# Kernel tuning notes

Hardware: AMD Instinct MI355X
Metric: run time of the kernel (lower is better)

## Reference

```python
import jax, jax.numpy as jnp
import numpy as np

NUM_TOKENS = 8192
TOKEN_DIM = 256
COMMITMENT_COST = 0.25
BATCH, SEQ = 32, 1024


def setup_inputs() -> dict:
    key = jax.random.key(0)
    k_z, k_cb = jax.random.split(key)
    z = jax.random.normal(k_z, (BATCH, SEQ, TOKEN_DIM), dtype=jnp.float32)
    # nn.Parameter(torch.randn(num_tokens, token_dim) * 0.02)
    codebook = jax.random.normal(k_cb, (NUM_TOKENS, TOKEN_DIM), dtype=jnp.float32) * 0.02
    return {"z": z, "codebook": codebook}


def reference(z, codebook):
    """VQ forward (eval mode): cdist^2 + argmin + gather + straight-through + commitment loss.

    z:        (B, S, D) continuous features
    codebook: (K, D) codebook vectors
    Returns (z_q, token_ids, loss) matching AudioCodebook.forward.
    """
    B, S, D = z.shape
    z_flat = z.reshape(-1, D)  # (N, D)
    # squared euclidean distances: ||z||^2 - 2 z.c^T + ||c||^2  -> (N, K)
    distances = (
        jnp.sum(z_flat * z_flat, axis=1, keepdims=True)
        - 2.0 * jnp.matmul(z_flat, codebook.T)
        + jnp.sum(codebook * codebook, axis=1)[None, :]
    )
    token_ids = jnp.argmin(distances, axis=-1)  # (N,)
    z_q = codebook[token_ids]  # (N, D) gather
    # straight-through estimator
    z_q_flat = z_flat + jax.lax.stop_gradient(z_q - z_flat)
    # commitment loss: mse(z_q_flat, stop_grad(z_flat))
    diff = z_q_flat - jax.lax.stop_gradient(z_flat)
    loss = COMMITMENT_COST * jnp.mean(diff * diff)
    return z_q_flat.reshape(B, S, D), token_ids.reshape(B, S), loss
```

## Files before the change

kernel.cpp:

```cpp
#include <hip/hip_runtime.h>
#include <math.h>

#define NTOK 32768
#define DIM 256
#define KCB 8192
#define RESCUE_TAU 4e-3f
#define RPASS 8

typedef _Float16 half8 __attribute__((ext_vector_type(8)));
typedef float f32x4 __attribute__((ext_vector_type(4)));
typedef unsigned long long u64;
typedef unsigned int u32;

#define OFF_AN    0ull
#define OFF_CN    131072ull
#define OFF_IDS   163840ull
#define OFF_RCNT  294912ull
#define OFF_RLIST 295040ull
#define OFF_PART  426112ull
#define OFF_PK1   442496ull
#define OFF_PV2   2539648ull
#define OFF_Z16   3588224ull
#define OFF_CB16  37142656ull
#define WS_NEED   45531264ull

#define GLOAD_LDS16(gp, lp) __builtin_amdgcn_global_load_lds( \
    (const __attribute__((address_space(1))) void*)(gp), \
    (__attribute__((address_space(3))) void*)(lp), 16, 0, 0)

static __device__ __forceinline__ u64 umin64(u64 a, u64 b) { return a < b ? a : b; }
static __device__ __forceinline__ u64 umax64(u64 a, u64 b) { return a < b ? b : a; }

__global__ __launch_bounds__(256)
void rownorm256_np(const float* __restrict__ M, float* __restrict__ out, int rows) {
  int r = blockIdx.x * 256 + threadIdx.x;
  if (r >= rows) return;
  const float* p = M + (size_t)r * DIM;
  float blk[2];
#pragma unroll
  for (int b = 0; b < 2; ++b) {
    const float* a = p + b * 128;
    float rr[8];
#pragma unroll
    for (int j = 0; j < 8; ++j) rr[j] = __fmul_rn(a[j], a[j]);
    for (int i = 8; i < 128; i += 8) {
#pragma unroll
      for (int j = 0; j < 8; ++j)
        rr[j] = __fadd_rn(rr[j], __fmul_rn(a[i + j], a[i + j]));
    }
    float s01 = __fadd_rn(rr[0], rr[1]);
    float s23 = __fadd_rn(rr[2], rr[3]);
    float s45 = __fadd_rn(rr[4], rr[5]);
    float s67 = __fadd_rn(rr[6], rr[7]);
    blk[b] = __fadd_rn(__fadd_rn(s01, s23), __fadd_rn(s45, s67));
  }
  out[r] = __fadd_rn(blk[0], blk[1]);
}

__global__ __launch_bounds__(128)
void conv_z16(const float* __restrict__ z, _Float16* __restrict__ dst) {
  const int tile = blockIdx.x >> 3, ks = blockIdx.x & 7, row = threadIdx.x;
  const float* src = z + ((size_t)(tile * 128 + row)) * DIM + ks * 32;
  _Float16* d = dst + (u64)tile * 65536 + (u64)ks * 8192 + row * 64;
  const int rs = row & 7;
#pragma unroll
  for (int q = 0; q < 4; ++q) {
    half8 hv, lv;
#pragma unroll
    for (int j = 0; j < 8; ++j) {
      float f = src[q * 8 + j] * 64.0f;
      _Float16 h = (_Float16)f;
      float lf = f - (float)h;
      hv[j] = h; lv[j] = (_Float16)lf;
    }
    *reinterpret_cast<half8*>(d + ((q ^ rs) * 8)) = hv;
    *reinterpret_cast<half8*>(d + (((q + 4) ^ rs) * 8)) = lv;
  }
}

__global__ __launch_bounds__(256)
void conv_cb16(const float* __restrict__ cb, _Float16* __restrict__ dst) {
  const int tile = blockIdx.x >> 3, ks = blockIdx.x & 7, row = threadIdx.x;
  const float* src = cb + ((size_t)(tile * 256 + row)) * DIM + ks * 32;
  _Float16* d = dst + (u64)tile * 131072 + (u64)ks * 16384 + row * 64;
  const int rs = row & 7;
#pragma unroll
  for (int q = 0; q < 4; ++q) {
    half8 hv, lv;
#pragma unroll
    for (int j = 0; j < 8; ++j) {
      float f = src[q * 8 + j] * 1024.0f;
      _Float16 h = (_Float16)f;
      float lf = f - (float)h;
      hv[j] = h; lv[j] = (_Float16)lf;
    }
    *reinterpret_cast<half8*>(d + ((q ^ rs) * 8)) = hv;
    *reinterpret_cast<half8*>(d + (((q + 4) ^ rs) * 8)) = lv;
  }
}

__global__ __launch_bounds__(256, 3)
void vq_mfma_top2(const _Float16* __restrict__ z16, const _Float16* __restrict__ cb16,
                  const float* __restrict__ An, const float* __restrict__ Cn,
                  u64* __restrict__ pk1, float* __restrict__ pv2) {
  __shared__ _Float16 Bs0[128 * 64];
  __shared__ _Float16 Bs1[128 * 64];
  __shared__ float    Cs[1024];
  __shared__ u64      t2k[64][2];
  __shared__ u32      t2v[64][2];

  const int tid = threadIdx.x;
  const int lane = tid & 63, w = tid >> 6;
  const int wm = w >> 1, wn = w & 1;
  const int swz = (blockIdx.x & 7) * 512 + (blockIdx.x >> 3);
  const int cg = swz >> 9, rem = swz & 511;
  const int ttile = rem >> 1, thalf = rem & 1;
  const int laneM = lane & 15, laneK = lane >> 4;
  const _Float16* zt = z16 + (u64)ttile * 65536;

  int offA[2];
#pragma unroll
  for (int f = 0; f < 2; ++f) {
    int row = thalf * 64 + wm * 32 + f * 16 + laneM;
    offA[f] = row * 64 + ((laneK ^ (row & 7)) * 8);
  }
  int offBh[4], offBl[4];
#pragma unroll
  for (int g = 0; g < 4; ++g) {
    int row = wn * 64 + g * 16 + laneM;
    offBh[g] = row * 64 + ((laneK ^ (row & 7)) * 8);
    offBl[g] = row * 64 + (((laneK + 4) ^ (row & 7)) * 8);
  }

  half8 Ah[8][2];
#pragma unroll
  for (int ks = 0; ks < 8; ++ks)
#pragma unroll
    for (int f = 0; f < 2; ++f)
      Ah[ks][f] = *reinterpret_cast<const half8*>(zt + ks * 8192 + offA[f]);

  float Areg[2][4];
#pragma unroll
  for (int f = 0; f < 2; ++f) {
    float4 a4 = *reinterpret_cast<const float4*>(
        &An[ttile * 128 + thalf * 64 + wm * 32 + f * 16 + laneK * 4]);
    Areg[f][0] = a4.x; Areg[f][1] = a4.y; Areg[f][2] = a4.z; Areg[f][3] = a4.w;
  }
  {
    float4 c4 = *reinterpret_cast<const float4*>(&Cn[cg * 1024 + tid * 4]);
    *reinterpret_cast<float4*>(&Cs[tid * 4]) = c4;
  }

  u32 v1b[8], v2b[8], c1v[8];
#pragma unroll
  for (int s = 0; s < 8; ++s) { v1b[s] = 0x7F800000u; v2b[s] = 0x7F800000u; c1v[s] = 0; }
  u32 codeSub = (u32)(cg * 1024 + wn * 64 + laneM);

#define STAGE_B(s, Bd) do {                                                  \
    const int ns_ = (s) >> 3, nk_ = (s) & 7;                                 \
    const _Float16* sb_ = cb16 + (u64)(cg * 4 + (ns_ >> 1)) * 131072 +       \
                          (u64)nk_ * 16384 + (u64)(ns_ & 1) * 8192 + tid * 8;\
    GLOAD_LDS16(sb_,        &Bd[tid * 8]);                                   \
    GLOAD_LDS16(sb_ + 2048, &Bd[tid * 8 + 2048]);                            \
    GLOAD_LDS16(sb_ + 4096, &Bd[tid * 8 + 4096]);                            \
    GLOAD_LDS16(sb_ + 6144, &Bd[tid * 8 + 6144]);                            \
  } while (0)

#define COMPUTE_KS(kc, Bsrc) do {                                            \
    _Pragma("unroll")                                                        \
    for (int g_ = 0; g_ < 4; ++g_) {                                         \
      half8 bh = *reinterpret_cast<const half8*>(&Bsrc[offBh[g_]]);          \
      half8 bl = *reinterpret_cast<const half8*>(&Bsrc[offBl[g_]]);          \
      _Pragma("unroll")                                                      \
      for (int f_ = 0; f_ < 2; ++f_)                                         \
        acc[f_][g_] = __builtin_amdgcn_mfma_f32_16x16x32_f16(Ah[kc][f_], bh, acc[f_][g_], 0, 0, 0); \
      _Pragma("unroll")                                                      \
      for (int f_ = 0; f_ < 2; ++f_)                                         \
        acc[f_][g_] = __builtin_amdgcn_mfma_f32_16x16x32_f16(Ah[kc][f_], bl, acc[f_][g_], 0, 0, 0); \
    }                                                                        \
  } while (0)

  STAGE_B(0, Bs0);
  __syncthreads();

  f32x4 acc[2][4];
#pragma unroll
  for (int f = 0; f < 2; ++f)
#pragma unroll
    for (int g = 0; g < 4; ++g) acc[f][g] = (f32x4){0.f, 0.f, 0.f, 0.f};

  for (int sub = 0; sub < 8; ++sub) {
#pragma unroll
    for (int ks = 0; ks < 8; ++ks) {
      const int step = sub * 8 + ks;
      if (step < 63) {
        if (ks & 1) STAGE_B(step + 1, Bs0);
        else        STAGE_B(step + 1, Bs1);
      }
      if (ks & 1) COMPUTE_KS(ks, Bs1);
      else        COMPUTE_KS(ks, Bs0);

      if (ks == 7) {
        const int cbase = sub * 128 + wn * 64 + laneM;
        float Cg[4];
#pragma unroll
        for (int g = 0; g < 4; ++g) Cg[g] = Cs[cbase + g * 16];
#pragma unroll
        for (int f = 0; f < 2; ++f) {
#pragma unroll
          for (int r = 0; r < 4; ++r) {
            const int sl = f * 4 + r;
            const float Ar = Areg[f][r];
#pragma unroll
            for (int g = 0; g < 4; ++g) {
              float p2 = __fmul_rn(acc[f][g][r], 0x1p-15f);
              float t1 = __fsub_rn(Ar, p2);
              float t  = __fadd_rn(t1, Cg[g]);
              u32 tb = __float_as_uint(t);
              u32 code = codeSub + (u32)(g * 16);
              bool lt1 = tb < v1b[sl];
              bool lt2 = tb < v2b[sl];
              v2b[sl] = lt1 ? v1b[sl] : (lt2 ? tb : v2b[sl]);
              c1v[sl] = lt1 ? code : c1v[sl];
              v1b[sl] = lt1 ? tb : v1b[sl];
            }
          }
        }
        codeSub += 128;
#pragma unroll
        for (int f = 0; f < 2; ++f)
#pragma unroll
          for (int g = 0; g < 4; ++g) acc[f][g] = (f32x4){0.f, 0.f, 0.f, 0.f};
      }
      __syncthreads();
    }
  }

#undef STAGE_B
#undef COMPUTE_KS

#pragma unroll
  for (int sl = 0; sl < 8; ++sl) {
#pragma unroll
    for (int d = 1; d < 16; d <<= 1) {
      u32 o1 = (u32)__shfl_xor((int)v1b[sl], d);
      u32 oc = (u32)__shfl_xor((int)c1v[sl], d);
      u32 o2 = (u32)__shfl_xor((int)v2b[sl], d);
      u64 k  = ((u64)v1b[sl] << 32) | c1v[sl];
      u64 ko = ((u64)o1 << 32) | oc;
      u32 loser = v1b[sl] < o1 ? o1 : v1b[sl];
      u32 nv2 = min(loser, min(v2b[sl], o2));
      u64 nk = umin64(k, ko);
      v1b[sl] = (u32)(nk >> 32); c1v[sl] = (u32)nk; v2b[sl] = nv2;
    }
  }
  if (laneM == 0) {
#pragma unroll
    for (int f = 0; f < 2; ++f)
#pragma unroll
      for (int r = 0; r < 4; ++r) {
        const int tloc = wm * 32 + f * 16 + laneK * 4 + r;
        const int sl = f * 4 + r;
        t2k[tloc][wn] = ((u64)v1b[sl] << 32) | c1v[sl];
        t2v[tloc][wn] = v2b[sl];
      }
  }
  __syncthreads();
  if (tid < 64) {
    u64 k0 = t2k[tid][0], k1 = t2k[tid][1];
    u32 va = t2v[tid][0], vb = t2v[tid][1];
    u64 K1 = umin64(k0, k1);
    u32 loser = (u32)(umax64(k0, k1) >> 32);
    u32 V2 = min(min(va, vb), loser);
    const int token = ttile * 128 + thalf * 64 + tid;
    pk1[(size_t)token * 8 + cg] = K1;
    pv2[(size_t)token * 8 + cg] = __uint_as_float(V2);
  }
}

__global__ __launch_bounds__(256)
void vq_detect(const u64* __restrict__ pk1, const float* __restrict__ pv2,
               int* __restrict__ ids, int* __restrict__ rcnt, int* __restrict__ rlist) {
  const int token = blockIdx.x * 256 + threadIdx.x;
  u64 K1 = pk1[(size_t)token * 8];
  float V2 = pv2[(size_t)token * 8];
#pragma unroll
  for (int c = 1; c < 8; ++c) {
    u64 k1 = pk1[(size_t)token * 8 + c];
    float v2 = pv2[(size_t)token * 8 + c];
    u64 n1 = (k1 < K1) ? k1 : K1;
    u64 hi = (k1 < K1) ? K1 : k1;
    float loser = __uint_as_float((unsigned)(hi >> 32));
    V2 = fminf(fminf(V2, v2), loser);
    K1 = n1;
  }
  ids[token] = (int)(K1 & 0xffffffffull);
  float d1 = __uint_as_float((unsigned)(K1 >> 32));
  if (V2 - d1 < RESCUE_TAU) {
    int p = atomicAdd(rcnt, 1);
    rlist[p] = token;
  }
}

__global__ __launch_bounds__(256)
void vq_rescue(const float* __restrict__ z, const float* __restrict__ cb,
               const float* __restrict__ An, const float* __restrict__ Cn,
               const int* __restrict__ rcnt, const int* __restrict__ rlist,
               int* __restrict__ ids) {
  __shared__ float zrow[RPASS][256];
  __shared__ u64 red[256];
  const int tid = threadIdx.x;
  const int total = *rcnt;
  for (int base = blockIdx.x * RPASS; base < total; base += gridDim.x * RPASS) {
    const int np = min(RPASS, total - base);
    __syncthreads();
    for (int li = tid; li < np * 256; li += 256)
      zrow[li >> 8][li & 255] = z[(size_t)rlist[base + (li >> 8)] * DIM + (li & 255)];
    __syncthreads();
    float Atok[RPASS];
#pragma unroll
    for (int s = 0; s < RPASS; ++s) Atok[s] = (s < np) ? An[rlist[base + s]] : 0.f;
    u64 bkey[RPASS];
#pragma unroll
    for (int s = 0; s < RPASS; ++s) bkey[s] = ~0ull;
    for (int jj = 0; jj < KCB / 256; ++jj) {
      const int j = jj * 256 + tid;
      const float4* crow = reinterpret_cast<const float4*>(cb + (size_t)j * DIM);
      float dots[RPASS];
#pragma unroll
      for (int s = 0; s < RPASS; ++s) dots[s] = 0.f;
      for (int k4 = 0; k4 < 64; ++k4) {
        const float4 c4 = crow[k4];
#pragma unroll
        for (int s = 0; s < RPASS; ++s) {
          const float4 z4 = *reinterpret_cast<const float4*>(&zrow[s][k4 * 4]);
          dots[s] = fmaf(z4.x, c4.x, dots[s]);
          dots[s] = fmaf(z4.y, c4.y, dots[s]);
          dots[s] = fmaf(z4.z, c4.z, dots[s]);
          dots[s] = fmaf(z4.w, c4.w, dots[s]);
        }
      }
      const float Cj = Cn[j];
#pragma unroll
      for (int s = 0; s < RPASS; ++s) {
        float p2 = __fmul_rn(2.0f, dots[s]);
        float t1 = __fsub_rn(Atok[s], p2);
        float t  = __fadd_rn(t1, Cj);
        u64 key = ((u64)__float_as_uint(t) << 32) | (u64)j;
        if (key < bkey[s]) bkey[s] = key;
      }
    }
    for (int s = 0; s < np; ++s) {
      __syncthreads();
      red[tid] = bkey[s];
      __syncthreads();
      for (int off = 128; off > 0; off >>= 1) {
        if (tid < off) { u64 o = red[tid + off]; if (o < red[tid]) red[tid] = o; }
        __syncthreads();
      }
      if (tid == 0) ids[rlist[base + s]] = (int)(red[0] & 0xffffffffull);
    }
  }
}

__global__ __launch_bounds__(256)
void vq_finalize_ids(const float* __restrict__ z, const float* __restrict__ cb,
                     const int* __restrict__ ids, float* __restrict__ out,
                     double* __restrict__ part) {
  __shared__ double sred[4];
  const int g64 = threadIdx.x >> 6, lane = threadIdx.x & 63;
  double s = 0.0;
#pragma unroll
  for (int i = 0; i < 4; ++i) {
    const int n = blockIdx.x * 16 + i * 4 + g64;
    const int bk = ids[n];
    const float4 c4 = *reinterpret_cast<const float4*>(&cb[(size_t)bk * DIM + lane * 4]);
    const float4 z4 = *reinterpret_cast<const float4*>(&z[(size_t)n * DIM + lane * 4]);
    *reinterpret_cast<float4*>(&out[(size_t)n * DIM + lane * 4]) = c4;
    float dx = __fsub_rn(c4.x, z4.x), dy = __fsub_rn(c4.y, z4.y);
    float dz = __fsub_rn(c4.z, z4.z), dw = __fsub_rn(c4.w, z4.w);
    s += (double)dx * dx + (double)dy * dy + (double)dz * dz + (double)dw * dw;
    if (lane == 0) out[(size_t)NTOK * DIM + n] = (float)bk;
  }
#pragma unroll
  for (int off = 32; off > 0; off >>= 1) s += __shfl_down(s, off);
  if (lane == 0) sred[g64] = s;
  __syncthreads();
  if (threadIdx.x == 0)
    part[blockIdx.x] = (sred[0] + sred[1]) + (sred[2] + sred[3]);
}

__global__ __launch_bounds__(256)
void vq_loss_write(const double* __restrict__ part, float* __restrict__ out) {
  __shared__ double red[256];
  double s = 0.0;
  for (int i = threadIdx.x; i < 2048; i += 256) s += part[i];
  red[threadIdx.x] = s;
  __syncthreads();
  for (int off = 128; off > 0; off >>= 1) {
    if (threadIdx.x < off) red[threadIdx.x] += red[threadIdx.x + off];
    __syncthreads();
  }
  if (threadIdx.x == 0)
    out[(size_t)NTOK * DIM + NTOK] =
        (float)(0.25 * red[0] / (double)((size_t)NTOK * DIM));
}

#define NCHUNK 8
#define CHUNK 1024
#define TT 128
#define CT 128
#define DC 32

__global__ __launch_bounds__(256)
void vq_argmin_kernel(const float* __restrict__ z, const float* __restrict__ cb,
                      const float* __restrict__ An, const float* __restrict__ Cn,
                      float* __restrict__ pv, int* __restrict__ pk) {
  __shared__ float zs[DC * TT];
  __shared__ float cs[DC * CT];
  const int tid = threadIdx.x;
  const int tx = tid & 15, ty = tid >> 4;
  const int chunk = blockIdx.x & 7;
  const int tile = blockIdx.x >> 3;
  const int base_t = tile * TT;
  const int base_k = chunk * CHUNK;
  float Areg[8];
#pragma unroll
  for (int i = 0; i < 8; ++i) Areg[i] = An[base_t + ty * 8 + i];
  float bestv[8]; int bestk[8];
#pragma unroll
  for (int i = 0; i < 8; ++i) { bestv[i] = INFINITY; bestk[i] = 0; }
  for (int st = 0; st < CHUNK / CT; ++st) {
    const int kb0 = base_k + st * CT;
    float acc[8][8];
#pragma unroll
    for (int i = 0; i < 8; ++i)
#pragma unroll
      for (int j = 0; j < 8; ++j) acc[i][j] = 0.f;
    for (int dc = 0; dc < DIM / DC; ++dc) {
      __syncthreads();
#pragma unroll
      for (int li = tid; li < DC * TT / 4; li += 256) {
        const int row = li >> 3;
        const int dv = li & 7;
        const int ibase = dv * 4 * 128 + (row ^ (dv << 2) ^ ((row & 32) >> 3));
        float4 v = *reinterpret_cast<const float4*>(
            &z[(size_t)(base_t + row) * DIM + dc * DC + dv * 4]);
        zs[ibase] = v.x; zs[ibase + 128] = v.y;
        zs[ibase + 256] = v.z; zs[ibase + 384] = v.w;
        float4 c = *reinterpret_cast<const float4*>(
            &cb[(size_t)(kb0 + row) * DIM + dc * DC + dv * 4]);
        cs[ibase] = c.x; cs[ibase + 128] = c.y;
        cs[ibase + 256] = c.z; cs[ibase + 384] = c.w;
      }
      __syncthreads();
#pragma unroll
      for (int dd = 0; dd < DC / 4; ++dd) {
        const int s1 = dd << 2;
        const float* zp0 = &zs[dd * 4 * 128 + ((ty * 8) ^ s1 ^ (ty & 4))];
        const float* zp1 = &zs[dd * 4 * 128 + ((ty * 8 + 4) ^ s1 ^ (ty & 4))];
        const float* cp0 = &cs[dd * 4 * 128 + ((tx * 8) ^ s1 ^ (tx & 4))];
        const float* cp1 = &cs[dd * 4 * 128 + ((tx * 8 + 4) ^ s1 ^ (tx & 4))];
#pragma unroll
        for (int q = 0; q < 4; ++q) {
          const float4 za  = *reinterpret_cast<const float4*>(zp0 + q * 128);
          const float4 zb  = *reinterpret_cast<const float4*>(zp1 + q * 128);
          const float4 ca  = *reinterpret_cast<const float4*>(cp0 + q * 128);
          const float4 cbv = *reinterpret_cast<const float4*>(cp1 + q * 128);
          const float zv[8] = {za.x, za.y, za.z, za.w, zb.x, zb.y, zb.z, zb.w};
          const float cv[8] = {ca.x, ca.y, ca.z, ca.w, cbv.x, cbv.y, cbv.z, cbv.w};
#pragma unroll
          for (int i = 0; i < 8; ++i)
#pragma unroll
            for (int j = 0; j < 8; ++j)
              acc[i][j] = fmaf(zv[i], cv[j], acc[i][j]);
        }
      }
    }
#pragma unroll
    for (int j = 0; j < 8; ++j) {
      const int klocal = st * CT + tx * 8 + j;
      const float Ck = Cn[base_k + klocal];
#pragma unroll
      for (int i = 0; i < 8; ++i) {
        float p2 = __fmul_rn(2.0f, acc[i][j]);
        float t1 = __fsub_rn(Areg[i], p2);
        float t  = __fadd_rn(t1, Ck);
        if (t < bestv[i]) { bestv[i] = t; bestk[i] = klocal; }
      }
    }
  }
  __syncthreads();
  float (*mv)[16] = reinterpret_cast<float(*)[16]>(zs);
  int   (*mk)[16] = reinterpret_cast<int(*)[16]>(zs + TT * 16);
#pragma unroll
  for (int i = 0; i < 8; ++i) { mv[ty * 8 + i][tx] = bestv[i]; mk[ty * 8 + i][tx] = bestk[i]; }
  __syncthreads();
  if (tid < TT) {
    float bv = mv[tid][0]; int bk = mk[tid][0];
#pragma unroll
    for (int x = 1; x < 16; ++x) {
      float v = mv[tid][x]; int k = mk[tid][x];
      if (v < bv || (v == bv && k < bk)) { bv = v; bk = k; }
    }
    size_t idx = (size_t)(base_t + tid) * NCHUNK + chunk;
    pv[idx] = bv;
    pk[idx] = base_k + bk;
  }
}

__global__ __launch_bounds__(256)
void vq_finalize(const float* __restrict__ z, const float* __restrict__ cb,
                 const float* __restrict__ pv, const int* __restrict__ pk,
                 float* __restrict__ out, double* __restrict__ loss_acc) {
  const int n = blockIdx.x * 4 + (threadIdx.x >> 6);
  const int lane = threadIdx.x & 63;
  float bv = INFINITY; int bk = 0;
#pragma unroll
  for (int c = 0; c < NCHUNK; ++c) {
    float v = pv[(size_t)n * NCHUNK + c];
    int k = pk[(size_t)n * NCHUNK + c];
    if (v < bv || (v == bv && k < bk)) { bv = v; bk = k; }
  }
  const float4 c4 = *reinterpret_cast<const float4*>(&cb[(size_t)bk * DIM + lane * 4]);
  const float4 z4 = *reinterpret_cast<const float4*>(&z[(size_t)n * DIM + lane * 4]);
  *reinterpret_cast<float4*>(&out[(size_t)n * DIM + lane * 4]) = c4;
  float dx = __fsub_rn(c4.x, z4.x), dy = __fsub_rn(c4.y, z4.y);
  float dz = __fsub_rn(c4.z, z4.z), dw = __fsub_rn(c4.w, z4.w);
  double s = (double)dx * dx + (double)dy * dy + (double)dz * dz + (double)dw * dw;
#pragma unroll
  for (int off = 32; off > 0; off >>= 1) s += __shfl_down(s, off);
  if (lane == 0) {
    out[(size_t)NTOK * DIM + n] = (float)bk;
    atomicAdd(loss_acc, s);
  }
}

__global__ void vq_loss_write_fb(const double* __restrict__ loss_acc, float* __restrict__ out) {
  out[(size_t)NTOK * DIM + NTOK] = (float)(0.25 * (*loss_acc) / (double)((size_t)NTOK * DIM));
}

extern "C" void kernel_launch(void* const* d_in, const int* in_sizes, int n_in,
                              void* d_out, int out_size, void* d_ws, size_t ws_size,
                              hipStream_t stream) {
  const float* z  = (const float*)d_in[0];
  const float* cb = (const float*)d_in[1];
  float* out = (float*)d_out;
  char* ws = (char*)d_ws;

  if (ws_size >= WS_NEED) {
    float*     An   = (float*)(ws + OFF_AN);
    float*     Cn   = (float*)(ws + OFF_CN);
    int*       ids  = (int*)(ws + OFF_IDS);
    int*       rcnt = (int*)(ws + OFF_RCNT);
    int*       rlist= (int*)(ws + OFF_RLIST);
    double*    part = (double*)(ws + OFF_PART);
    u64*       pk1  = (u64*)(ws + OFF_PK1);
    float*     pv2  = (float*)(ws + OFF_PV2);
    _Float16*  z16  = (_Float16*)(ws + OFF_Z16);
    _Float16*  c16  = (_Float16*)(ws + OFF_CB16);

    hipMemsetAsync(rcnt, 0, 128, stream);
    rownorm256_np<<<NTOK / 256, 256, 0, stream>>>(z, An, NTOK);
    rownorm256_np<<<KCB / 256, 256, 0, stream>>>(cb, Cn, KCB);
    conv_z16<<<256 * 8, 128, 0, stream>>>(z, z16);
    conv_cb16<<<32 * 8, 256, 0, stream>>>(cb, c16);
    vq_mfma_top2<<<4096, 256, 0, stream>>>(z16, c16, An, Cn, pk1, pv2);
    vq_detect<<<NTOK / 256, 256, 0, stream>>>(pk1, pv2, ids, rcnt, rlist);
    vq_rescue<<<1024, 256, 0, stream>>>(z, cb, An, Cn, rcnt, rlist, ids);
    vq_finalize_ids<<<NTOK / 16, 256, 0, stream>>>(z, cb, ids, out, part);
    vq_loss_write<<<1, 256, 0, stream>>>(part, out);
  } else {
    float*  An = (float*)(ws);
    float*  Cn = (float*)(ws + 131072);
    float*  pv = (float*)(ws + 163840);
    int*    pk = (int*)(ws + 1212416);
    double* loss = (double*)(ws + 2260992);
    hipMemsetAsync(loss, 0, sizeof(double), stream);
    rownorm256_np<<<NTOK / 256, 256, 0, stream>>>(z, An, NTOK);
    rownorm256_np<<<KCB / 256, 256, 0, stream>>>(cb, Cn, KCB);
    vq_argmin_kernel<<<(NTOK / TT) * NCHUNK, 256, 0, stream>>>(z, cb, An, Cn, pv, pk);
    vq_finalize<<<NTOK / 4, 256, 0, stream>>>(z, cb, pv, pk, out, loss);
    vq_loss_write_fb<<<1, 1, 0, stream>>>(loss, out);
  }
}
```

Measured before the change: 689.4 us.

## Split rescue pass across codebook chunks with wave-shuffle reduction and atomicMin

```diff
diff --git a/kernel.cpp b/kernel.cpp
--- a/kernel.cpp
+++ b/kernel.cpp
@@ -5,7 +5,6 @@
 #define DIM 256
 #define KCB 8192
 #define RESCUE_TAU 4e-3f
-#define RPASS 8
 
 typedef _Float16 half8 __attribute__((ext_vector_type(8)));
 typedef float f32x4 __attribute__((ext_vector_type(4)));
@@ -303,63 +302,65 @@
 }
 
 __global__ __launch_bounds__(256)
-void vq_rescue(const float* __restrict__ z, const float* __restrict__ cb,
-               const float* __restrict__ An, const float* __restrict__ Cn,
-               const int* __restrict__ rcnt, const int* __restrict__ rlist,
-               int* __restrict__ ids) {
-  __shared__ float zrow[RPASS][256];
-  __shared__ u64 red[256];
+void vq_rescue2(const float* __restrict__ z, const float* __restrict__ cb,
+                const float* __restrict__ An, const float* __restrict__ Cn,
+                const int* __restrict__ rcnt, const int* __restrict__ rlist,
+                u64* __restrict__ rmin) {
   const int tid = threadIdx.x;
   const int total = *rcnt;
-  for (int base = blockIdx.x * RPASS; base < total; base += gridDim.x * RPASS) {
-    const int np = min(RPASS, total - base);
-    __syncthreads();
-    for (int li = tid; li < np * 256; li += 256)
-      zrow[li >> 8][li & 255] = z[(size_t)rlist[base + (li >> 8)] * DIM + (li & 255)];
-    __syncthreads();
-    float Atok[RPASS];
-#pragma unroll
-    for (int s = 0; s < RPASS; ++s) Atok[s] = (s < np) ? An[rlist[base + s]] : 0.f;
-    u64 bkey[RPASS];
-#pragma unroll
-    for (int s = 0; s < RPASS; ++s) bkey[s] = ~0ull;
-    for (int jj = 0; jj < KCB / 256; ++jj) {
-      const int j = jj * 256 + tid;
-      const float4* crow = reinterpret_cast<const float4*>(cb + (size_t)j * DIM);
-      float dots[RPASS];
-#pragma unroll
-      for (int s = 0; s < RPASS; ++s) dots[s] = 0.f;
-      for (int k4 = 0; k4 < 64; ++k4) {
-        const float4 c4 = crow[k4];
-#pragma unroll
-        for (int s = 0; s < RPASS; ++s) {
-          const float4 z4 = *reinterpret_cast<const float4*>(&zrow[s][k4 * 4]);
-          dots[s] = fmaf(z4.x, c4.x, dots[s]);
-          dots[s] = fmaf(z4.y, c4.y, dots[s]);
-          dots[s] = fmaf(z4.z, c4.z, dots[s]);
-          dots[s] = fmaf(z4.w, c4.w, dots[s]);
-        }
-      }
-      const float Cj = Cn[j];
-#pragma unroll
-      for (int s = 0; s < RPASS; ++s) {
+  if (total == 0) return;
+  const int nb = (total + 31) >> 5;
+  for (int wi = blockIdx.x; wi < nb * 32; wi += gridDim.x) {
+    const int batch = wi >> 5, chunk = wi & 31;
+    const int base = batch * 32;
+    const int np = min(32, total - base);
+    int toks[32];
+#pragma unroll
+    for (int s = 0; s < 32; ++s)
+      toks[s] = rlist[base + (s < np ? s : 0)];
+    const int j = chunk * 256 + tid;
+    const float4* crow = reinterpret_cast<const float4*>(cb + (size_t)j * DIM);
+    float dots[32];
+#pragma unroll
+    for (int s = 0; s < 32; ++s) dots[s] = 0.f;
+    for (int k4 = 0; k4 < 64; ++k4) {
+      const float4 c4 = crow[k4];
+#pragma unroll
+      for (int s = 0; s < 32; ++s) {
+        const float4 z4 = *reinterpret_cast<const float4*>(
+            z + (size_t)toks[s] * DIM + k4 * 4);
+        dots[s] = fmaf(z4.x, c4.x, dots[s]);
+        dots[s] = fmaf(z4.y, c4.y, dots[s]);
+        dots[s] = fmaf(z4.z, c4.z, dots[s]);
+        dots[s] = fmaf(z4.w, c4.w, dots[s]);
+      }
+    }
+    const float Cj = Cn[j];
+#pragma unroll
+    for (int s = 0; s < 32; ++s) {
+      if (s < np) {
         float p2 = __fmul_rn(2.0f, dots[s]);
-        float t1 = __fsub_rn(Atok[s], p2);
+        float t1 = __fsub_rn(An[toks[s]], p2);
         float t  = __fadd_rn(t1, Cj);
         u64 key = ((u64)__float_as_uint(t) << 32) | (u64)j;
-        if (key < bkey[s]) bkey[s] = key;
-      }
-    }
-    for (int s = 0; s < np; ++s) {
-      __syncthreads();
-      red[tid] = bkey[s];
-      __syncthreads();
-      for (int off = 128; off > 0; off >>= 1) {
-        if (tid < off) { u64 o = red[tid + off]; if (o < red[tid]) red[tid] = o; }
-        __syncthreads();
-      }
-      if (tid == 0) ids[rlist[base + s]] = (int)(red[0] & 0xffffffffull);
-    }
+#pragma unroll
+        for (int d = 1; d < 64; d <<= 1) {
+          u64 o = __shfl_xor(key, d);
+          key = o < key ? o : key;
+        }
+        if ((tid & 63) == 0) atomicMin(&rmin[toks[s]], key);
+      }
+    }
+  }
+}
+
+__global__ __launch_bounds__(256)
+void vq_rescue_apply(const int* __restrict__ rcnt, const int* __restrict__ rlist,
+                     const u64* __restrict__ rmin, int* __restrict__ ids) {
+  const int total = *rcnt;
+  for (int i = blockIdx.x * 256 + threadIdx.x; i < total; i += gridDim.x * 256) {
+    const int t = rlist[i];
+    ids[t] = (int)(rmin[t] & 0xffffffffull);
   }
 }
 
@@ -559,6 +560,7 @@
     float*     pv2  = (float*)(ws + OFF_PV2);
     _Float16*  z16  = (_Float16*)(ws + OFF_Z16);
     _Float16*  c16  = (_Float16*)(ws + OFF_CB16);
+    u64*       rmin = pk1;
 
     hipMemsetAsync(rcnt, 0, 128, stream);
     rownorm256_np<<<NTOK / 256, 256, 0, stream>>>(z, An, NTOK);
@@ -567,7 +569,9 @@
     conv_cb16<<<32 * 8, 256, 0, stream>>>(cb, c16);
     vq_mfma_top2<<<4096, 256, 0, stream>>>(z16, c16, An, Cn, pk1, pv2);
     vq_detect<<<NTOK / 256, 256, 0, stream>>>(pk1, pv2, ids, rcnt, rlist);
-    vq_rescue<<<1024, 256, 0, stream>>>(z, cb, An, Cn, rcnt, rlist, ids);
+    hipMemsetAsync(rmin, 0xFF, (size_t)NTOK * sizeof(u64), stream);
+    vq_rescue2<<<2048, 256, 0, stream>>>(z, cb, An, Cn, rcnt, rlist, rmin);
+    vq_rescue_apply<<<32, 256, 0, stream>>>(rcnt, rlist, rmin, ids);
     vq_finalize_ids<<<NTOK / 16, 256, 0, stream>>>(z, cb, ids, out, part);
     vq_loss_write<<<1, 256, 0, stream>>>(part, out);
   } else {
```

Measured after the change: 575.6 us (median of 2 runs). -16.5%, faster.
